# Kernel tuning notes

Measured on AMD Instinct MI355X. Metric: run time of the kernel, lower is better.

The kernel has to match this reference:

```python
import jax, jax.numpy as jnp
import numpy as np

EPS = 1e-5
RADIUS = 1.0

def bn(x, gamma, beta, axis=1):
    # inference-mode BatchNorm1d: running_mean=0, running_var=1
    shape = [1] * x.ndim
    shape[axis] = -1
    return x * (gamma / jnp.sqrt(1.0 + EPS)).reshape(shape) + beta.reshape(shape)

def pconv(x, w):
    # pointwise Conv1d (kernel_size=1): x [B,Cin,N], w [Cout,Cin]
    return jnp.einsum('oi,bin->bon', w, x)

def sq_dist(a, b):
    # a [B,N,3], b [B,S,3] -> squared pairwise distances [B,N,S]
    return (jnp.sum(a * a, -1)[:, :, None] + jnp.sum(b * b, -1)[:, None, :]
            - 2.0 * jnp.einsum('bnc,bsc->bns', a, b))

def index_points(points, idx):
    # points [B,S,...], idx [B,...] -> gathered [B, idx.shape[1:], ...]
    return jax.vmap(lambda p, i: p[i])(points, idx)

def fps(xyz, npoint):
    # farthest point sampling (deterministic start at index 0)
    B, N, _ = xyz.shape
    binds = jnp.arange(B)
    def step(carry, _):
        dist, far = carry
        c = xyz[binds, far]                                    # [B,3]
        d = jnp.sum((xyz - c[:, None, :]) ** 2, -1)            # [B,N]
        dist = jnp.minimum(dist, d)
        nxt = jnp.argmax(dist, -1).astype(jnp.int32)
        return (dist, nxt), far
    init = (jnp.full((B, N), 1e10, xyz.dtype), jnp.zeros((B,), jnp.int32))
    _, idx = jax.lax.scan(step, init, None, length=npoint)
    return jnp.transpose(idx)                                   # [B,npoint]

def query_ball(radius, nsample, xyz, new_xyz):
    # indices of first nsample points within radius of each center
    B, N, _ = xyz.shape
    S = new_xyz.shape[1]
    d2 = sq_dist(new_xyz, xyz)                                  # [B,S,N]
    gidx = jnp.broadcast_to(jnp.arange(N, dtype=jnp.int32), (B, S, N))
    gidx = jnp.where(d2 > radius * radius, N, gidx)
    gidx = jnp.sort(gidx, axis=-1)[:, :, :nsample]
    first = gidx[:, :, :1]
    gidx = jnp.where(gidx == N, first, gidx)
    return jnp.clip(gidx, 0, N - 1)

def sample_and_group(npoint, nsample, radius, xyz, points):
    fps_idx = fps(xyz, npoint)
    new_xyz = index_points(xyz, fps_idx)                        # [B,S,3]
    new_pts = index_points(points, fps_idx)                     # [B,S,D]
    idx = query_ball(radius, nsample, xyz, new_xyz)             # [B,S,K]
    grouped = index_points(points, idx)                         # [B,S,K,D]
    centered = grouped - new_pts[:, :, None, :]
    rep = jnp.broadcast_to(new_pts[:, :, None, :], centered.shape)
    return new_xyz, jnp.concatenate([centered, rep], axis=-1)   # [B,S,K,2D]

def local_op(x, w1, g1, b1, w2, g2, b2):
    # x [B,n,K,d]; shared pointwise MLP over channels then max over K
    h = jnp.einsum('oi,bnki->bnok', w1, x)
    h = jax.nn.relu(bn(h, g1, b1, axis=2))
    h = jnp.einsum('oi,bnik->bnok', w2, h)
    h = jax.nn.relu(bn(h, g2, b2, axis=2))
    return jnp.transpose(jnp.max(h, -1), (0, 2, 1))             # [B,out,n]

def feature_prop(xyz1, xyz2, points1, points2, w1, g1, b1, w2, g2, b2):
    # 3-NN inverse-distance interpolation of points2 onto xyz1, concat points1
    p1 = jnp.transpose(xyz1, (0, 2, 1))                         # [B,N,3]
    p2 = jnp.transpose(xyz2, (0, 2, 1))                         # [B,S,3]
    f2 = jnp.transpose(points2, (0, 2, 1))                      # [B,S,D2]
    negd, idx = jax.lax.top_k(-sq_dist(p1, p2), 3)              # [B,N,3]
    recip = 1.0 / (-negd + 1e-8)
    w = recip / jnp.sum(recip, -1, keepdims=True)
    interp = jnp.sum(index_points(f2, idx) * w[..., None], 2)   # [B,N,D2]
    new = jnp.concatenate([points1, jnp.transpose(interp, (0, 2, 1))], axis=1)
    new = jax.nn.relu(bn(pconv(new, w1), g1, b1))
    new = jax.nn.relu(bn(pconv(new, w2), g2, b2))
    return new


def setup_inputs() -> dict:
    key = jax.random.key(0)
    ks = iter(jax.random.split(key, 80))
    def W(*s):  return jax.random.normal(next(ks), s, jnp.float32) * 0.05
    def G(n):   return 1.0 + 0.1 * jax.random.normal(next(ks), (n,), jnp.float32)
    def Bt(n):  return 0.1 * jax.random.normal(next(ks), (n,), jnp.float32)
    inp = {"x": jax.random.uniform(next(ks), (4, 8192, 3), jnp.float32)}
    inp.update(w_emb1=W(64, 3), g_emb1=G(64), be_emb1=Bt(64),
               w_emb2=W(64, 64), g_emb2=G(64), be_emb2=Bt(64),
               l0_w1=W(128, 128), l0_g1=G(128), l0_b1=Bt(128),
               l0_w2=W(128, 128), l0_g2=G(128), l0_b2=Bt(128),
               l1_w1=W(256, 256), l1_g1=G(256), l1_b1=Bt(256),
               l1_w2=W(256, 256), l1_g2=G(256), l1_b2=Bt(256),
               f0_w1=W(256, 384), f0_g1=G(256), f0_b1=Bt(256),
               f0_w2=W(512, 256), f0_g2=G(512), f0_b2=Bt(512),
               f1_w1=W(512, 576), f1_g1=G(512), f1_b1=Bt(512),
               f1_w2=W(1024, 512), f1_g2=G(1024), f1_b2=Bt(1024),
               c1_w=W(512, 1024), c1_bias=Bt(512), c1_g=G(512), c1_beta=Bt(512),
               c2_w=W(128, 512), c2_bias=Bt(128), c2_g=G(128), c2_beta=Bt(128),
               out_w=W(8, 128), out_bias=Bt(8))
    return inp


def reference(x, w_emb1, g_emb1, be_emb1, w_emb2, g_emb2, be_emb2,
              l0_w1, l0_g1, l0_b1, l0_w2, l0_g2, l0_b2,
              l1_w1, l1_g1, l1_b1, l1_w2, l1_g2, l1_b2,
              f0_w1, f0_g1, f0_b1, f0_w2, f0_g2, f0_b2,
              f1_w1, f1_g1, f1_b1, f1_w2, f1_g2, f1_b2,
              c1_w, c1_bias, c1_g, c1_beta, c2_w, c2_bias, c2_g, c2_beta,
              out_w, out_bias):
    xyz = x                                                     # [B,N,3]
    h = jnp.transpose(x, (0, 2, 1))                             # [B,3,N]
    h = jax.nn.relu(bn(pconv(h, w_emb1), g_emb1, be_emb1))
    h = jax.nn.relu(bn(pconv(h, w_emb2), g_emb2, be_emb2))
    feats0 = h                                                  # [B,64,N]
    xyz1, g1f = sample_and_group(2048, 32, RADIUS, xyz, jnp.transpose(h, (0, 2, 1)))
    feats1 = local_op(g1f, l0_w1, l0_g1, l0_b1, l0_w2, l0_g2, l0_b2)   # [B,128,2048]
    xyz2, g2f = sample_and_group(1024, 32, RADIUS, xyz1, jnp.transpose(feats1, (0, 2, 1)))
    feats2 = local_op(g2f, l1_w1, l1_g1, l1_b1, l1_w2, l1_g2, l1_b2)   # [B,256,1024]
    h = feature_prop(jnp.transpose(xyz1, (0, 2, 1)), jnp.transpose(xyz2, (0, 2, 1)),
                     feats1, feats2, f0_w1, f0_g1, f0_b1, f0_w2, f0_g2, f0_b2)   # [B,512,2048]
    h = feature_prop(jnp.transpose(xyz, (0, 2, 1)), jnp.transpose(xyz1, (0, 2, 1)),
                     feats0, h, f1_w1, f1_g1, f1_b1, f1_w2, f1_g2, f1_b2)        # [B,1024,N]
    h = jax.nn.relu(bn(pconv(h, c1_w) + c1_bias[None, :, None], c1_g, c1_beta))
    h = jax.nn.relu(bn(pconv(h, c2_w) + c2_bias[None, :, None], c2_g, c2_beta))
    logits = pconv(h, out_w) + out_bias[None, :, None]
    return jnp.transpose(logits, (0, 2, 1))                     # [B,N,labels]
```

## Files before the change

kernel.cpp:

```cpp
#include <hip/hip_runtime.h>
#include <math.h>


static constexpr size_t O_FEATS0 = 0;
static constexpr size_t O_FEATS1 = 8388608;
static constexpr size_t O_FEATS2 = 12582912;
static constexpr size_t O_FP0OUT = 16777216;
static constexpr size_t O_XYZ1   = 33554432;
static constexpr size_t O_XYZ2   = 33652736;
static constexpr size_t O_FPS1   = 33701888;
static constexpr size_t O_FPS2   = 33734656;
static constexpr size_t O_BALL1  = 33751040;
static constexpr size_t O_BALL2  = 34799616;
static constexpr size_t O_NN0I   = 35323904;
static constexpr size_t O_NN0W   = 35422208;
static constexpr size_t O_NN1I   = 35520512;
static constexpr size_t O_NN1W   = 35913728;
static constexpr size_t O_REG0   = 36306944;
static constexpr size_t O_REG1   = 103415808;
static constexpr size_t WS_NEED  = 170524672;

typedef float v2f __attribute__((ext_vector_type(2)));

__device__ __forceinline__ unsigned long long u64max(unsigned long long a,
                                                     unsigned long long b) {
  return a > b ? a : b;
}
template <int CTRL>
__device__ __forceinline__ unsigned long long dpp_step(unsigned long long k) {
  const int lo = (int)(unsigned)k;
  const int hi = (int)(unsigned)(k >> 32);
  const int nlo = __builtin_amdgcn_update_dpp(lo, lo, CTRL, 0xf, 0xf, false);
  const int nhi = __builtin_amdgcn_update_dpp(hi, hi, CTRL, 0xf, 0xf, false);
  return ((unsigned long long)(unsigned)nhi << 32) | (unsigned)nlo;
}

template <int N, int NP>
__device__ void fps_core(const float* __restrict__ xyz, int* __restrict__ out,
                         float* __restrict__ oxyz, float* sx, float* sy,
                         float* sz, int* sfar, unsigned long long* skey,
                         int b, int t) {
  #pragma clang fp contract(off)
  constexpr int PPT = N / 256;
  constexpr int PAIRS = PPT / 2;
  const float* xb = xyz + (size_t)b * N * 3;
  for (int i = t; i < N; i += 256) {
    sx[i] = xb[i * 3 + 0];
    sy[i] = xb[i * 3 + 1];
    sz[i] = xb[i * 3 + 2];
  }
  __syncthreads();
  v2f px[PAIRS], py[PAIRS], pz[PAIRS], ds[PAIRS];
  #pragma unroll
  for (int k = 0; k < PAIRS; ++k) {
    const int g = t * PPT + 2 * k;
    px[k].x = sx[g]; px[k].y = sx[g + 1];
    py[k].x = sy[g]; py[k].y = sy[g + 1];
    pz[k].x = sz[g]; pz[k].y = sz[g + 1];
    ds[k].x = 1e10f; ds[k].y = 1e10f;
  }
  const int wid = t >> 6, lane = t & 63;
  int far = 0;
  float ccx = sx[0], ccy = sy[0], ccz = sz[0];
  for (int it = 0; it < NP; ++it) {
    if (t == 0) sfar[it] = far;
    v2f cx2, cy2, cz2;
    cx2.x = ccx; cx2.y = ccx;
    cy2.x = ccy; cy2.y = ccy;
    cz2.x = ccz; cz2.y = ccz;
    #pragma unroll
    for (int k = 0; k < PAIRS; ++k) {
      const v2f dx = px[k] - cx2;
      const v2f dy = py[k] - cy2;
      const v2f dz = pz[k] - cz2;
      const v2f d = dx * dx + dy * dy + dz * dz;
      v2f nd;
      nd.x = fminf(ds[k].x, d.x);
      nd.y = fminf(ds[k].y, d.y);
      ds[k] = nd;
    }
    v2f tv[PAIRS / 2];
    #pragma unroll
    for (int k = 0; k < PAIRS / 2; ++k) {
      tv[k].x = fmaxf(ds[k].x, ds[k + PAIRS / 2].x);
      tv[k].y = fmaxf(ds[k].y, ds[k + PAIRS / 2].y);
    }
    #pragma unroll
    for (int w = PAIRS / 4; w >= 1; w >>= 1) {
      #pragma unroll
      for (int k = 0; k < w; ++k) {
        tv[k].x = fmaxf(tv[k].x, tv[k + w].x);
        tv[k].y = fmaxf(tv[k].y, tv[k + w].y);
      }
    }
    const float bv = fmaxf(tv[0].x, tv[0].y);
    unsigned mask = 0u;
    #pragma unroll
    for (int k = 0; k < PAIRS; ++k) {
      mask |= (ds[k].x == bv) ? (1u << (2 * k)) : 0u;
      mask |= (ds[k].y == bv) ? (1u << (2 * k + 1)) : 0u;
    }
    const int bjl = __builtin_ctz(mask);
    unsigned long long bk =
        ((unsigned long long)__float_as_uint(bv) << 32) |
        (unsigned long long)(unsigned)(~(unsigned)(t * PPT + bjl));
    bk = u64max(bk, dpp_step<0x111>(bk));
    bk = u64max(bk, dpp_step<0x112>(bk));
    bk = u64max(bk, dpp_step<0x114>(bk));
    bk = u64max(bk, dpp_step<0x118>(bk));
    bk = u64max(bk, dpp_step<0x142>(bk));
    bk = u64max(bk, dpp_step<0x143>(bk));
    const int p = it & 1;
    if (lane == 63) skey[p * 4 + wid] = bk;
    __syncthreads();
    unsigned long long wk = skey[p * 4 + 0];
    #pragma unroll
    for (int q = 1; q < 4; ++q) {
      const unsigned long long k2 = skey[p * 4 + q];
      wk = (k2 > wk) ? k2 : wk;
    }
    far = (int)(~(unsigned)wk);
    ccx = sx[far]; ccy = sy[far]; ccz = sz[far];
  }
  __syncthreads();
  for (int i = t; i < NP; i += 256) {
    const int n = sfar[i];
    out[(size_t)b * NP + i] = n;
    oxyz[((size_t)b * NP + i) * 3 + 0] = sx[n];
    oxyz[((size_t)b * NP + i) * 3 + 1] = sy[n];
    oxyz[((size_t)b * NP + i) * 3 + 2] = sz[n];
  }
}

template <int N, int NP>
__global__ __launch_bounds__(256, 1) void fps_emb_kernel(
    const float* __restrict__ xyz, int* __restrict__ out,
    float* __restrict__ oxyz, const float* __restrict__ w1,
    const float* __restrict__ g1, const float* __restrict__ b1,
    const float* __restrict__ w2, const float* __restrict__ g2,
    const float* __restrict__ b2, float* __restrict__ femb) {
  __shared__ float sx[N], sy[N], sz[N];
  __shared__ int sfar[NP];
  __shared__ unsigned long long skey[8];
  if (blockIdx.x >= 4) {
    const int bid = blockIdx.x - 4;
    const int t = threadIdx.x;
    const int o = t & 63, pl = t >> 6;
    const int pt = bid * 4 + pl;
    const float x0 = xyz[(size_t)pt * 3 + 0];
    const float x1 = xyz[(size_t)pt * 3 + 1];
    const float x2 = xyz[(size_t)pt * 3 + 2];
    const float SQ = sqrtf(1.0f + 1e-5f);
    float v = w1[o * 3 + 0] * x0 + w1[o * 3 + 1] * x1 + w1[o * 3 + 2] * x2;
    v = fmaxf(v * (g1[o] / SQ) + b1[o], 0.0f);
    float* h = sx;
    h[pl * 64 + o] = v;
    __syncthreads();
    float acc = 0.0f;
    #pragma unroll 8
    for (int i = 0; i < 64; ++i) acc += w2[o * 64 + i] * h[pl * 64 + i];
    float y = fmaxf(acc * (g2[o] / SQ) + b2[o], 0.0f);
    femb[(size_t)pt * 64 + o] = y;
    return;
  }
  fps_core<N, NP>(xyz, out, oxyz, sx, sy, sz, sfar, skey, blockIdx.x,
                  threadIdx.x);
}

__global__ __launch_bounds__(256, 1) void ballnnfps_kernel(
    const float* __restrict__ cloud, const float* __restrict__ ctr,
    int* __restrict__ ballOut, int sbits, int N, int nBallBlk,
    const float* __restrict__ txyz, const float* __restrict__ sxyz,
    int* __restrict__ oi, float* __restrict__ ow, int s1bits, int S2,
    const float* __restrict__ fxyz, int* __restrict__ fout,
    float* __restrict__ foxyz) {
  __shared__ __align__(16) char smem[28800];
  const int t = threadIdx.x;
  if ((int)blockIdx.x < 4) {
    unsigned long long* skey = (unsigned long long*)smem;
    int* sfar = (int*)(smem + 64);
    float* sx = (float*)(smem + 64 + 4096);
    float* sy = sx + 2048;
    float* sz = sy + 2048;
    fps_core<2048, 1024>(fxyz, fout, foxyz, sx, sy, sz, sfar, skey,
                         blockIdx.x, t);
    return;
  }
  if ((int)blockIdx.x < 4 + nBallBlk) {
    int* lists = (int*)smem;
    const int lane = t & 63, wid = t >> 6;
    const int wg = (blockIdx.x - 4) * 4 + wid;
    const int b = wg >> sbits;
    const float cx = ctr[(size_t)wg * 3 + 0];
    const float cy = ctr[(size_t)wg * 3 + 1];
    const float cz = ctr[(size_t)wg * 3 + 2];
    const float an = __fadd_rn(__fadd_rn(__fmul_rn(cx, cx), __fmul_rn(cy, cy)),
                               __fmul_rn(cz, cz));
    int fill = 0;
    for (int ch = 0; ch < (N >> 6) && fill < 32; ++ch) {
      const int n = ch * 64 + lane;
      const float bx = cloud[((size_t)b * N + n) * 3 + 0];
      const float by = cloud[((size_t)b * N + n) * 3 + 1];
      const float bz = cloud[((size_t)b * N + n) * 3 + 2];
      const float bb = __fadd_rn(
          __fadd_rn(__fmul_rn(bx, bx), __fmul_rn(by, by)), __fmul_rn(bz, bz));
      const float dot = __fadd_rn(
          __fadd_rn(__fmul_rn(cx, bx), __fmul_rn(cy, by)), __fmul_rn(cz, bz));
      const float d2 = __fsub_rn(__fadd_rn(an, bb), __fmul_rn(2.0f, dot));
      const bool q = (d2 <= 1.0f);
      const unsigned long long mask = __ballot(q);
      if (q) {
        const int pos = fill + __popcll(mask & ((1ull << lane) - 1ull));
        if (pos < 32) lists[wid * 32 + pos] = n;
      }
      fill += (int)__popcll(mask);
    }
    __syncthreads();
    if (lane < 32) {
      int v = lists[wid * 32 + 0];
      if (lane < fill) v = lists[wid * 32 + lane];
      ballOut[(size_t)wg * 32 + lane] = v;
    }
    return;
  }
  float* ss = (float*)smem;
  const int row = (blockIdx.x - 4 - nBallBlk) * 256 + t;
  const int b = row >> s1bits;
  for (int i = t; i < S2 * 3; i += 256) ss[i] = sxyz[(size_t)b * S2 * 3 + i];
  __syncthreads();
  const float ax = txyz[(size_t)row * 3 + 0];
  const float ay = txyz[(size_t)row * 3 + 1];
  const float az = txyz[(size_t)row * 3 + 2];
  const float an = __fadd_rn(__fadd_rn(__fmul_rn(ax, ax), __fmul_rn(ay, ay)),
                             __fmul_rn(az, az));
  float d0 = 3.4e38f, d1 = 3.4e38f, d2v = 3.4e38f;
  int i0 = 0, i1 = 0, i2 = 0;
  for (int j = 0; j < S2; ++j) {
    const float bx = ss[j * 3 + 0], by = ss[j * 3 + 1], bz = ss[j * 3 + 2];
    const float bb = __fadd_rn(__fadd_rn(__fmul_rn(bx, bx), __fmul_rn(by, by)),
                               __fmul_rn(bz, bz));
    const float dot = __fadd_rn(__fadd_rn(__fmul_rn(ax, bx), __fmul_rn(ay, by)),
                                __fmul_rn(az, bz));
    const float dd = __fsub_rn(__fadd_rn(an, bb), __fmul_rn(2.0f, dot));
    if (dd < d0) {
      d2v = d1; i2 = i1; d1 = d0; i1 = i0; d0 = dd; i0 = j;
    } else if (dd < d1) {
      d2v = d1; i2 = i1; d1 = dd; i1 = j;
    } else if (dd < d2v) {
      d2v = dd; i2 = j;
    }
  }
  const float r0 = 1.0f / (d0 + 1e-8f);
  const float r1 = 1.0f / (d1 + 1e-8f);
  const float r2 = 1.0f / (d2v + 1e-8f);
  const float sum = __fadd_rn(__fadd_rn(r0, r1), r2);
  oi[(size_t)row * 3 + 0] = i0;
  oi[(size_t)row * 3 + 1] = i1;
  oi[(size_t)row * 3 + 2] = i2;
  ow[(size_t)row * 3 + 0] = r0 / sum;
  ow[(size_t)row * 3 + 1] = r1 / sum;
  ow[(size_t)row * 3 + 2] = r2 / sum;
}

__global__ __launch_bounds__(256) void ballnn_kernel(
    const float* __restrict__ cloud, const float* __restrict__ ctr,
    int* __restrict__ ballOut, int sbits, int N, int nBallBlk,
    const float* __restrict__ txyz, const float* __restrict__ sxyz,
    int* __restrict__ oi, float* __restrict__ ow, int s1bits, int S2) {
  __shared__ int lists[4][32];
  __shared__ float ss[6144];
  const int t = threadIdx.x;
  if ((int)blockIdx.x < nBallBlk) {
    const int lane = t & 63, wid = t >> 6;
    const int wg = blockIdx.x * 4 + wid;
    const int b = wg >> sbits;
    const float cx = ctr[(size_t)wg * 3 + 0];
    const float cy = ctr[(size_t)wg * 3 + 1];
    const float cz = ctr[(size_t)wg * 3 + 2];
    const float an = __fadd_rn(__fadd_rn(__fmul_rn(cx, cx), __fmul_rn(cy, cy)),
                               __fmul_rn(cz, cz));
    int fill = 0;
    for (int ch = 0; ch < (N >> 6) && fill < 32; ++ch) {
      const int n = ch * 64 + lane;
      const float bx = cloud[((size_t)b * N + n) * 3 + 0];
      const float by = cloud[((size_t)b * N + n) * 3 + 1];
      const float bz = cloud[((size_t)b * N + n) * 3 + 2];
      const float bb = __fadd_rn(
          __fadd_rn(__fmul_rn(bx, bx), __fmul_rn(by, by)), __fmul_rn(bz, bz));
      const float dot = __fadd_rn(
          __fadd_rn(__fmul_rn(cx, bx), __fmul_rn(cy, by)), __fmul_rn(cz, bz));
      const float d2 = __fsub_rn(__fadd_rn(an, bb), __fmul_rn(2.0f, dot));
      const bool q = (d2 <= 1.0f);
      const unsigned long long mask = __ballot(q);
      if (q) {
        const int pos = fill + __popcll(mask & ((1ull << lane) - 1ull));
        if (pos < 32) lists[wid][pos] = n;
      }
      fill += (int)__popcll(mask);
    }
    __syncthreads();
    if (lane < 32) {
      int v = lists[wid][0];
      if (lane < fill) v = lists[wid][lane];
      ballOut[(size_t)wg * 32 + lane] = v;
    }
    return;
  }
  const int row = (blockIdx.x - nBallBlk) * 256 + t;
  const int b = row >> s1bits;
  for (int i = t; i < S2 * 3; i += 256) ss[i] = sxyz[(size_t)b * S2 * 3 + i];
  __syncthreads();
  const float ax = txyz[(size_t)row * 3 + 0];
  const float ay = txyz[(size_t)row * 3 + 1];
  const float az = txyz[(size_t)row * 3 + 2];
  const float an = __fadd_rn(__fadd_rn(__fmul_rn(ax, ax), __fmul_rn(ay, ay)),
                             __fmul_rn(az, az));
  float d0 = 3.4e38f, d1 = 3.4e38f, d2v = 3.4e38f;
  int i0 = 0, i1 = 0, i2 = 0;
  for (int j = 0; j < S2; ++j) {
    const float bx = ss[j * 3 + 0], by = ss[j * 3 + 1], bz = ss[j * 3 + 2];
    const float bb = __fadd_rn(__fadd_rn(__fmul_rn(bx, bx), __fmul_rn(by, by)),
                               __fmul_rn(bz, bz));
    const float dot = __fadd_rn(__fadd_rn(__fmul_rn(ax, bx), __fmul_rn(ay, by)),
                                __fmul_rn(az, bz));
    const float dd = __fsub_rn(__fadd_rn(an, bb), __fmul_rn(2.0f, dot));
    if (dd < d0) {
      d2v = d1; i2 = i1; d1 = d0; i1 = i0; d0 = dd; i0 = j;
    } else if (dd < d1) {
      d2v = d1; i2 = i1; d1 = dd; i1 = j;
    } else if (dd < d2v) {
      d2v = dd; i2 = j;
    }
  }
  const float r0 = 1.0f / (d0 + 1e-8f);
  const float r1 = 1.0f / (d1 + 1e-8f);
  const float r2 = 1.0f / (d2v + 1e-8f);
  const float sum = __fadd_rn(__fadd_rn(r0, r1), r2);
  oi[(size_t)row * 3 + 0] = i0;
  oi[(size_t)row * 3 + 1] = i1;
  oi[(size_t)row * 3 + 2] = i2;
  ow[(size_t)row * 3 + 0] = r0 / sum;
  ow[(size_t)row * 3 + 1] = r1 / sum;
  ow[(size_t)row * 3 + 2] = r2 / sum;
}

#define CMAP(c) ((((c) >> 3) * 12) + ((c) & 7))

__global__ __launch_bounds__(256) void conv_gather_kernel(
    const float* __restrict__ f, const int* __restrict__ ball,
    const int* __restrict__ fps, int g0, int Cf, int sbits, int Npts,
    const float* __restrict__ W, float* __restrict__ Y, int O,
    const float* __restrict__ gamma, const float* __restrict__ beta) {
  const int C = Cf * 2;
  __shared__ float Xs[16][188];
  __shared__ float Ws[16][188];
  const int t = threadIdx.x;
  const size_t m0 = (size_t)blockIdx.x * 128;
  const int o0 = blockIdx.y * 128;
  const int r0 = t >> 2;
  const int cq0 = (t & 3) * 4;
  const int mq = t & 15, nq = t >> 4;
  const int ca = CMAP(r0), cb = CMAP(r0 + 64);
  const int mA = (int)m0 + r0, mB = (int)m0 + r0 + 64;
  const int glA = g0 + (mA >> 5), glB = g0 + (mB >> 5);
  const int srcA = ball[(size_t)glA * 32 + (mA & 31)];
  const int srcB = ball[(size_t)glB * 32 + (mB & 31)];
  const int ctrA = fps[glA], ctrB = fps[glB];
  const float* fbA = f + (size_t)(glA >> sbits) * Npts * Cf;
  const float* fbB = f + (size_t)(glB >> sbits) * Npts * Cf;
  v2f acc[8][4];
  #pragma unroll
  for (int i = 0; i < 8; ++i)
    #pragma unroll
    for (int j = 0; j < 4; ++j) acc[i][j] = (v2f){0.0f, 0.0f};

  for (int kk = 0; kk < C; kk += 16) {
    const int col = kk + cq0;
    const bool lo = col < Cf;
    const int col2 = lo ? col : col - Cf;
    float4 xa, xb;
    {
      const float4 c4 = *(const float4*)(fbA + (size_t)ctrA * Cf + col2);
      if (lo) {
        const float4 s4 = *(const float4*)(fbA + (size_t)srcA * Cf + col);
        xa = make_float4(s4.x - c4.x, s4.y - c4.y, s4.z - c4.z, s4.w - c4.w);
      } else {
        xa = c4;
      }
    }
    {
      const float4 c4 = *(const float4*)(fbB + (size_t)ctrB * Cf + col2);
      if (lo) {
        const float4 s4 = *(const float4*)(fbB + (size_t)srcB * Cf + col);
        xb = make_float4(s4.x - c4.x, s4.y - c4.y, s4.z - c4.z, s4.w - c4.w);
      } else {
        xb = c4;
      }
    }
    const float4 wa = *(const float4*)(W + (size_t)(o0 + r0) * C + kk + cq0);
    const float4 wb =
        *(const float4*)(W + (size_t)(o0 + r0 + 64) * C + kk + cq0);
    __syncthreads();
    Xs[cq0 + 0][ca] = xa.x; Xs[cq0 + 1][ca] = xa.y;
    Xs[cq0 + 2][ca] = xa.z; Xs[cq0 + 3][ca] = xa.w;
    Xs[cq0 + 0][cb] = xb.x; Xs[cq0 + 1][cb] = xb.y;
    Xs[cq0 + 2][cb] = xb.z; Xs[cq0 + 3][cb] = xb.w;
    Ws[cq0 + 0][ca] = wa.x; Ws[cq0 + 1][ca] = wa.y;
    Ws[cq0 + 2][ca] = wa.z; Ws[cq0 + 3][ca] = wa.w;
    Ws[cq0 + 0][cb] = wb.x; Ws[cq0 + 1][cb] = wb.y;
    Ws[cq0 + 2][cb] = wb.z; Ws[cq0 + 3][cb] = wb.w;
    __syncthreads();
    #pragma unroll
    for (int k = 0; k < 16; ++k) {
      const float4 a0 = *(const float4*)&Xs[k][mq * 12];
      const float4 a1 = *(const float4*)&Xs[k][mq * 12 + 4];
      const float4 b0 = *(const float4*)&Ws[k][nq * 12];
      const float4 b1 = *(const float4*)&Ws[k][nq * 12 + 4];
      const float am[8] = {a0.x, a0.y, a0.z, a0.w, a1.x, a1.y, a1.z, a1.w};
      v2f bv[4];
      bv[0] = (v2f){b0.x, b0.y};
      bv[1] = (v2f){b0.z, b0.w};
      bv[2] = (v2f){b1.x, b1.y};
      bv[3] = (v2f){b1.z, b1.w};
      #pragma unroll
      for (int i = 0; i < 8; ++i) {
        const v2f as = (v2f){am[i], am[i]};
        #pragma unroll
        for (int j = 0; j < 4; ++j) acc[i][j] += as * bv[j];
      }
    }
  }

  const float SQ = sqrtf(1.0f + 1e-5f);
  float s[8], sh[8];
  #pragma unroll
  for (int j = 0; j < 8; ++j) {
    const int o = o0 + nq * 8 + j;
    s[j] = gamma[o] / SQ;
    sh[j] = beta[o];
  }
  #pragma unroll
  for (int i = 0; i < 8; ++i) {
    float y[8];
    #pragma unroll
    for (int j = 0; j < 4; ++j) {
      y[2 * j] = fmaxf(acc[i][j].x * s[2 * j] + sh[2 * j], 0.0f);
      y[2 * j + 1] = fmaxf(acc[i][j].y * s[2 * j + 1] + sh[2 * j + 1], 0.0f);
    }
    const size_t off = (m0 + mq * 8 + i) * O + o0 + nq * 8;
    *(float4*)(Y + off) = make_float4(y[0], y[1], y[2], y[3]);
    *(float4*)(Y + off + 4) = make_float4(y[4], y[5], y[6], y[7]);
  }
}

__global__ __launch_bounds__(256) void conv2sm_kernel(
    const float* __restrict__ X, const float* __restrict__ W,
    float* __restrict__ F, int C, int O, const float* __restrict__ gamma,
    const float* __restrict__ beta) {
  __shared__ float Xs[16][188];
  __shared__ float Ws[16][188];
  const int t = threadIdx.x;
  const size_t m0 = (size_t)blockIdx.x * 128;
  const int o0 = blockIdx.y * 128;
  const int r0 = t >> 2;
  const int cq0 = (t & 3) * 4;
  const int mq = t & 15, nq = t >> 4;
  const int ca = CMAP(r0), cb = CMAP(r0 + 64);
  v2f acc[8][4];
  #pragma unroll
  for (int i = 0; i < 8; ++i)
    #pragma unroll
    for (int j = 0; j < 4; ++j) acc[i][j] = (v2f){0.0f, 0.0f};

  for (int kk = 0; kk < C; kk += 16) {
    const float4 xa = *(const float4*)(X + (m0 + r0) * C + kk + cq0);
    const float4 xb = *(const float4*)(X + (m0 + r0 + 64) * C + kk + cq0);
    const float4 wa = *(const float4*)(W + (size_t)(o0 + r0) * C + kk + cq0);
    const float4 wb =
        *(const float4*)(W + (size_t)(o0 + r0 + 64) * C + kk + cq0);
    __syncthreads();
    Xs[cq0 + 0][ca] = xa.x; Xs[cq0 + 1][ca] = xa.y;
    Xs[cq0 + 2][ca] = xa.z; Xs[cq0 + 3][ca] = xa.w;
    Xs[cq0 + 0][cb] = xb.x; Xs[cq0 + 1][cb] = xb.y;
    Xs[cq0 + 2][cb] = xb.z; Xs[cq0 + 3][cb] = xb.w;
    Ws[cq0 + 0][ca] = wa.x; Ws[cq0 + 1][ca] = wa.y;
    Ws[cq0 + 2][ca] = wa.z; Ws[cq0 + 3][ca] = wa.w;
    Ws[cq0 + 0][cb] = wb.x; Ws[cq0 + 1][cb] = wb.y;
    Ws[cq0 + 2][cb] = wb.z; Ws[cq0 + 3][cb] = wb.w;
    __syncthreads();
    #pragma unroll
    for (int k = 0; k < 16; ++k) {
      const float4 a0 = *(const float4*)&Xs[k][mq * 12];
      const float4 a1 = *(const float4*)&Xs[k][mq * 12 + 4];
      const float4 b0 = *(const float4*)&Ws[k][nq * 12];
      const float4 b1 = *(const float4*)&Ws[k][nq * 12 + 4];
      const float am[8] = {a0.x, a0.y, a0.z, a0.w, a1.x, a1.y, a1.z, a1.w};
      v2f bv[4];
      bv[0] = (v2f){b0.x, b0.y};
      bv[1] = (v2f){b0.z, b0.w};
      bv[2] = (v2f){b1.x, b1.y};
      bv[3] = (v2f){b1.z, b1.w};
      #pragma unroll
      for (int i = 0; i < 8; ++i) {
        const v2f as = (v2f){am[i], am[i]};
        #pragma unroll
        for (int j = 0; j < 4; ++j) acc[i][j] += as * bv[j];
      }
    }
  }

  const float SQ = sqrtf(1.0f + 1e-5f);
  float s[8], sh[8];
  #pragma unroll
  for (int j = 0; j < 8; ++j) {
    const int o = o0 + nq * 8 + j;
    s[j] = gamma[o] / SQ;
    sh[j] = beta[o];
  }
  float colmax[8];
  #pragma unroll
  for (int j = 0; j < 8; ++j) colmax[j] = -3.4e38f;
  #pragma unroll
  for (int i = 0; i < 8; ++i) {
    #pragma unroll
    for (int j = 0; j < 4; ++j) {
      const float va = fmaxf(acc[i][j].x * s[2 * j] + sh[2 * j], 0.0f);
      const float vb = fmaxf(acc[i][j].y * s[2 * j + 1] + sh[2 * j + 1], 0.0f);
      colmax[2 * j] = fmaxf(colmax[2 * j], va);
      colmax[2 * j + 1] = fmaxf(colmax[2 * j + 1], vb);
    }
  }
  __syncthreads();
  float* smax = &Xs[0][0];
  #pragma unroll
  for (int j = 0; j < 8; ++j) smax[mq * 132 + nq * 8 + j] = colmax[j];
  __syncthreads();
  #pragma unroll
  for (int q = 0; q < 2; ++q) {
    const int idx = t + q * 256;
    const int g = idx >> 7;
    const int col = idx & 127;
    const float m =
        fmaxf(fmaxf(smax[(4 * g + 0) * 132 + col], smax[(4 * g + 1) * 132 + col]),
              fmaxf(smax[(4 * g + 2) * 132 + col], smax[(4 * g + 3) * 132 + col]));
    F[(size_t)(blockIdx.x * 4 + g) * O + o0 + col] = m;
  }
}

__global__ __launch_bounds__(256) void conv_kernel(
    const float* __restrict__ X, const float* __restrict__ W,
    float* __restrict__ Y, int C, int O, const float* __restrict__ gamma,
    const float* __restrict__ beta, const float* __restrict__ bias, int relu) {
  __shared__ float Xs[16][188];
  __shared__ float Ws[16][188];
  const int t = threadIdx.x;
  const size_t m0 = (size_t)blockIdx.x * 128;
  const int o0 = blockIdx.y * 128;
  const int r0 = t >> 2;
  const int cq0 = (t & 3) * 4;
  const int mq = t & 15, nq = t >> 4;
  const int ca = CMAP(r0), cb = CMAP(r0 + 64);
  v2f acc[8][4];
  #pragma unroll
  for (int i = 0; i < 8; ++i)
    #pragma unroll
    for (int j = 0; j < 4; ++j) acc[i][j] = (v2f){0.0f, 0.0f};

  for (int kk = 0; kk < C; kk += 16) {
    const float4 xa = *(const float4*)(X + (m0 + r0) * C + kk + cq0);
    const float4 xb = *(const float4*)(X + (m0 + r0 + 64) * C + kk + cq0);
    const float4 wa = *(const float4*)(W + (size_t)(o0 + r0) * C + kk + cq0);
    const float4 wb =
        *(const float4*)(W + (size_t)(o0 + r0 + 64) * C + kk + cq0);
    __syncthreads();
    Xs[cq0 + 0][ca] = xa.x; Xs[cq0 + 1][ca] = xa.y;
    Xs[cq0 + 2][ca] = xa.z; Xs[cq0 + 3][ca] = xa.w;
    Xs[cq0 + 0][cb] = xb.x; Xs[cq0 + 1][cb] = xb.y;
    Xs[cq0 + 2][cb] = xb.z; Xs[cq0 + 3][cb] = xb.w;
    Ws[cq0 + 0][ca] = wa.x; Ws[cq0 + 1][ca] = wa.y;
    Ws[cq0 + 2][ca] = wa.z; Ws[cq0 + 3][ca] = wa.w;
    Ws[cq0 + 0][cb] = wb.x; Ws[cq0 + 1][cb] = wb.y;
    Ws[cq0 + 2][cb] = wb.z; Ws[cq0 + 3][cb] = wb.w;
    __syncthreads();
    #pragma unroll
    for (int k = 0; k < 16; ++k) {
      const float4 a0 = *(const float4*)&Xs[k][mq * 12];
      const float4 a1 = *(const float4*)&Xs[k][mq * 12 + 4];
      const float4 b0 = *(const float4*)&Ws[k][nq * 12];
      const float4 b1 = *(const float4*)&Ws[k][nq * 12 + 4];
      const float am[8] = {a0.x, a0.y, a0.z, a0.w, a1.x, a1.y, a1.z, a1.w};
      v2f bv[4];
      bv[0] = (v2f){b0.x, b0.y};
      bv[1] = (v2f){b0.z, b0.w};
      bv[2] = (v2f){b1.x, b1.y};
      bv[3] = (v2f){b1.z, b1.w};
      #pragma unroll
      for (int i = 0; i < 8; ++i) {
        const v2f as = (v2f){am[i], am[i]};
        #pragma unroll
        for (int j = 0; j < 4; ++j) acc[i][j] += as * bv[j];
      }
    }
  }

  const float SQ = sqrtf(1.0f + 1e-5f);
  float s[8], sh[8];
  #pragma unroll
  for (int j = 0; j < 8; ++j) {
    const int o = o0 + nq * 8 + j;
    const float sc = gamma ? (gamma[o] / SQ) : 1.0f;
    float bb = beta ? beta[o] : 0.0f;
    if (bias) bb = bb + bias[o] * sc;
    s[j] = sc; sh[j] = bb;
  }
  #pragma unroll
  for (int i = 0; i < 8; ++i) {
    float y[8];
    #pragma unroll
    for (int j = 0; j < 4; ++j) {
      float va = acc[i][j].x * s[2 * j] + sh[2 * j];
      float vb = acc[i][j].y * s[2 * j + 1] + sh[2 * j + 1];
      y[2 * j] = relu ? fmaxf(va, 0.0f) : va;
      y[2 * j + 1] = relu ? fmaxf(vb, 0.0f) : vb;
    }
    const size_t off = (m0 + mq * 8 + i) * O + o0 + nq * 8;
    *(float4*)(Y + off) = make_float4(y[0], y[1], y[2], y[3]);
    *(float4*)(Y + off + 4) = make_float4(y[4], y[5], y[6], y[7]);
  }
}

template <int CT, int C0, int CS2>
__global__ __launch_bounds__(256) void concat_interp_kernel(
    float* __restrict__ dst, const float* __restrict__ srcA,
    const float* __restrict__ srcB, const int* __restrict__ idx,
    const float* __restrict__ w, int s1bits, int S2) {
  const int id = blockIdx.x * 256 + threadIdx.x;
  constexpr int CPR = CT / 4;
  const int row = id / CPR;
  const int c4 = (id - row * CPR) * 4;
  if (c4 < C0) {
    const float4 v = *(const float4*)(srcA + (size_t)row * C0 + c4);
    *(float4*)(dst + (size_t)row * CT + c4) = v;
  } else {
    const int b = row >> s1bits;
    const int cc = c4 - C0;
    const int j0 = idx[(size_t)row * 3 + 0];
    const int j1 = idx[(size_t)row * 3 + 1];
    const int j2 = idx[(size_t)row * 3 + 2];
    const float w0 = w[(size_t)row * 3 + 0];
    const float w1 = w[(size_t)row * 3 + 1];
    const float w2 = w[(size_t)row * 3 + 2];
    const float4 f0 = *(const float4*)(srcB + ((size_t)b * S2 + j0) * CS2 + cc);
    const float4 f1 = *(const float4*)(srcB + ((size_t)b * S2 + j1) * CS2 + cc);
    const float4 f2 = *(const float4*)(srcB + ((size_t)b * S2 + j2) * CS2 + cc);
    float4 v;
    v.x = f0.x * w0 + f1.x * w1 + f2.x * w2;
    v.y = f0.y * w0 + f1.y * w1 + f2.y * w2;
    v.z = f0.z * w0 + f1.z * w1 + f2.z * w2;
    v.w = f0.w * w0 + f1.w * w1 + f2.w * w2;
    *(float4*)(dst + (size_t)row * CT + c4) = v;
  }
}

__global__ __launch_bounds__(256) void outfinal_kernel(
    const float* __restrict__ X, const float* __restrict__ Wt,
    const float* __restrict__ bias, float* __restrict__ out) {
  __shared__ float Xs[32][132];
  const int t = threadIdx.x;
  const int p0 = blockIdx.x * 32;
  #pragma unroll
  for (int q = 0; q < 4; ++q) {
    const int id = t + q * 256;
    const int r = id >> 5, c4 = (id & 31) * 4;
    const float4 v = *(const float4*)(X + (size_t)(p0 + r) * 128 + c4);
    Xs[r][c4 + 0] = v.x; Xs[r][c4 + 1] = v.y;
    Xs[r][c4 + 2] = v.z; Xs[r][c4 + 3] = v.w;
  }
  __syncthreads();
  const int p = t >> 3, o = t & 7;
  float acc = 0.0f;
  #pragma unroll 8
  for (int i = 0; i < 128; ++i) acc += Wt[o * 128 + i] * Xs[p][i];
  out[(size_t)(p0 + p) * 8 + o] = acc + bias[o];
}

extern "C" void kernel_launch(void* const* d_in, const int* in_sizes, int n_in,
                              void* d_out, int out_size, void* d_ws,
                              size_t ws_size, hipStream_t stream) {
  const float* x       = (const float*)d_in[0];
  const float* w_emb1  = (const float*)d_in[1];
  const float* g_emb1  = (const float*)d_in[2];
  const float* be_emb1 = (const float*)d_in[3];
  const float* w_emb2  = (const float*)d_in[4];
  const float* g_emb2  = (const float*)d_in[5];
  const float* be_emb2 = (const float*)d_in[6];
  const float* l0_w1 = (const float*)d_in[7];
  const float* l0_g1 = (const float*)d_in[8];
  const float* l0_b1 = (const float*)d_in[9];
  const float* l0_w2 = (const float*)d_in[10];
  const float* l0_g2 = (const float*)d_in[11];
  const float* l0_b2 = (const float*)d_in[12];
  const float* l1_w1 = (const float*)d_in[13];
  const float* l1_g1 = (const float*)d_in[14];
  const float* l1_b1 = (const float*)d_in[15];
  const float* l1_w2 = (const float*)d_in[16];
  const float* l1_g2 = (const float*)d_in[17];
  const float* l1_b2 = (const float*)d_in[18];
  const float* f0_w1 = (const float*)d_in[19];
  const float* f0_g1 = (const float*)d_in[20];
  const float* f0_b1 = (const float*)d_in[21];
  const float* f0_w2 = (const float*)d_in[22];
  const float* f0_g2 = (const float*)d_in[23];
  const float* f0_b2 = (const float*)d_in[24];
  const float* f1_w1 = (const float*)d_in[25];
  const float* f1_g1 = (const float*)d_in[26];
  const float* f1_b1 = (const float*)d_in[27];
  const float* f1_w2 = (const float*)d_in[28];
  const float* f1_g2 = (const float*)d_in[29];
  const float* f1_b2 = (const float*)d_in[30];
  const float* c1_w    = (const float*)d_in[31];
  const float* c1_bias = (const float*)d_in[32];
  const float* c1_g    = (const float*)d_in[33];
  const float* c1_beta = (const float*)d_in[34];
  const float* c2_w    = (const float*)d_in[35];
  const float* c2_bias = (const float*)d_in[36];
  const float* c2_g    = (const float*)d_in[37];
  const float* c2_beta = (const float*)d_in[38];
  const float* out_w    = (const float*)d_in[39];
  const float* out_bias = (const float*)d_in[40];

  if (ws_size < WS_NEED) return;

  char* ws = (char*)d_ws;
  float* feats0 = (float*)(ws + O_FEATS0);
  float* feats1 = (float*)(ws + O_FEATS1);
  float* feats2 = (float*)(ws + O_FEATS2);
  float* fp0out = (float*)(ws + O_FP0OUT);
  float* xyz1   = (float*)(ws + O_XYZ1);
  float* xyz2   = (float*)(ws + O_XYZ2);
  int*   fps1   = (int*)(ws + O_FPS1);
  int*   fps2   = (int*)(ws + O_FPS2);
  int*   ball1  = (int*)(ws + O_BALL1);
  int*   ball2  = (int*)(ws + O_BALL2);
  int*   nn0i   = (int*)(ws + O_NN0I);
  float* nn0w   = (float*)(ws + O_NN0W);
  int*   nn1i   = (int*)(ws + O_NN1I);
  float* nn1w   = (float*)(ws + O_NN1W);
  float* REG0   = (float*)(ws + O_REG0);
  float* REG1   = (float*)(ws + O_REG1);
  float* outp   = (float*)d_out;
  hipStream_t s = stream;

  fps_emb_kernel<8192, 2048><<<4 + 8192, 256, 0, s>>>(
      x, fps1, xyz1, w_emb1, g_emb1, be_emb1, w_emb2, g_emb2, be_emb2, feats0);

  ballnnfps_kernel<<<4 + 2048 + 128, 256, 0, s>>>(
      x, xyz1, ball1, 11, 8192, 2048, x, xyz1, nn1i, nn1w, 13, 2048,
      xyz1, fps2, xyz2);

  for (int c = 0; c < 2; ++c) {
    conv_gather_kernel<<<dim3(1024, 1), 256, 0, s>>>(
        feats0, ball1, fps1, c * 4096, 64, 11, 8192, l0_w1, REG1, 128, l0_g1,
        l0_b1);
    conv2sm_kernel<<<dim3(1024, 1), 256, 0, s>>>(
        REG1, l0_w2, feats1 + (size_t)c * 4096 * 128, 128, 128, l0_g2, l0_b2);
  }

  ballnn_kernel<<<1024 + 32, 256, 0, s>>>(xyz1, xyz2, ball2, 10, 2048, 1024,
                                          xyz1, xyz2, nn0i, nn0w, 11, 1024);

  for (int c = 0; c < 2; ++c) {
    conv_gather_kernel<<<dim3(512, 2), 256, 0, s>>>(
        feats1, ball2, fps2, c * 2048, 128, 10, 2048, l1_w1, REG1, 256, l1_g1,
        l1_b1);
    conv2sm_kernel<<<dim3(512, 2), 256, 0, s>>>(
        REG1, l1_w2, feats2 + (size_t)c * 2048 * 256, 256, 256, l1_g2, l1_b2);
  }

  concat_interp_kernel<384, 128, 256><<<3072, 256, 0, s>>>(
      REG0, feats1, feats2, nn0i, nn0w, 11, 1024);
  conv_kernel<<<dim3(64, 2), 256, 0, s>>>(REG0, f0_w1, REG1, 384, 256, f0_g1,
                                          f0_b1, nullptr, 1);
  conv_kernel<<<dim3(64, 4), 256, 0, s>>>(REG1, f0_w2, fp0out, 256, 512, f0_g2,
                                          f0_b2, nullptr, 1);

  for (int b = 0; b < 4; b += 2) {
    concat_interp_kernel<576, 64, 512><<<9216, 256, 0, s>>>(
        REG0, feats0 + (size_t)b * 8192 * 64, fp0out + (size_t)b * 2048 * 512,
        nn1i + (size_t)b * 8192 * 3, nn1w + (size_t)b * 8192 * 3, 13, 2048);
    conv_kernel<<<dim3(128, 4), 256, 0, s>>>(REG0, f1_w1, REG1, 576, 512,
                                             f1_g1, f1_b1, nullptr, 1);
    conv_kernel<<<dim3(128, 8), 256, 0, s>>>(REG1, f1_w2, REG0, 512, 1024,
                                             f1_g2, f1_b2, nullptr, 1);
    conv_kernel<<<dim3(128, 4), 256, 0, s>>>(REG0, c1_w, REG1, 1024, 512,
                                             c1_g, c1_beta, c1_bias, 1);
    conv_kernel<<<dim3(128, 1), 256, 0, s>>>(REG1, c2_w, REG0, 512, 128,
                                             c2_g, c2_beta, c2_bias, 1);
    outfinal_kernel<<<512, 256, 0, s>>>(REG0, out_w, out_bias,
                                        outp + (size_t)b * 8192 * 8);
  }
}
```

Before: 4.618 ms.

## Double-buffer shared-memory tiles in the three GEMM conv kernels

The three tiled fp32 GEMM kernels (gather-conv, conv+max, plain conv) now keep two shared-memory tile buffers. The global loads for the next K-slice are issued before computing on the current one. This removes one __syncthreads per iteration and hides global load latency behind the FMA loop. In exchange, shared memory per block doubles to about 48KB and register pressure rises from holding the prefetched values, which can lower occupancy.

```diff
diff --git a/kernel.cpp b/kernel.cpp
--- a/kernel.cpp
+++ b/kernel.cpp
@@ -346,14 +346,45 @@
 
 #define CMAP(c) ((((c) >> 3) * 12) + ((c) & 7))
 
+#define STORE_TILE(B)                                                   \
+  Xs[B][cq0 + 0][ca] = xa.x; Xs[B][cq0 + 1][ca] = xa.y;                 \
+  Xs[B][cq0 + 2][ca] = xa.z; Xs[B][cq0 + 3][ca] = xa.w;                 \
+  Xs[B][cq0 + 0][cb] = xb.x; Xs[B][cq0 + 1][cb] = xb.y;                 \
+  Xs[B][cq0 + 2][cb] = xb.z; Xs[B][cq0 + 3][cb] = xb.w;                 \
+  Ws[B][cq0 + 0][ca] = wa.x; Ws[B][cq0 + 1][ca] = wa.y;                 \
+  Ws[B][cq0 + 2][ca] = wa.z; Ws[B][cq0 + 3][ca] = wa.w;                 \
+  Ws[B][cq0 + 0][cb] = wb.x; Ws[B][cq0 + 1][cb] = wb.y;                 \
+  Ws[B][cq0 + 2][cb] = wb.z; Ws[B][cq0 + 3][cb] = wb.w;
+
+#define COMPUTE_TILE(B)                                                 \
+  _Pragma("unroll")                                                     \
+  for (int k = 0; k < 16; ++k) {                                        \
+    const float4 a0 = *(const float4*)&Xs[B][k][mq * 12];               \
+    const float4 a1 = *(const float4*)&Xs[B][k][mq * 12 + 4];           \
+    const float4 b0 = *(const float4*)&Ws[B][k][nq * 12];               \
+    const float4 b1 = *(const float4*)&Ws[B][k][nq * 12 + 4];           \
+    const float am[8] = {a0.x, a0.y, a0.z, a0.w, a1.x, a1.y, a1.z, a1.w}; \
+    v2f bv[4];                                                          \
+    bv[0] = (v2f){b0.x, b0.y};                                          \
+    bv[1] = (v2f){b0.z, b0.w};                                          \
+    bv[2] = (v2f){b1.x, b1.y};                                          \
+    bv[3] = (v2f){b1.z, b1.w};                                          \
+    _Pragma("unroll")                                                   \
+    for (int i = 0; i < 8; ++i) {                                       \
+      const v2f as = (v2f){am[i], am[i]};                               \
+      _Pragma("unroll")                                                 \
+      for (int j = 0; j < 4; ++j) acc[i][j] += as * bv[j];              \
+    }                                                                   \
+  }
+
 __global__ __launch_bounds__(256) void conv_gather_kernel(
     const float* __restrict__ f, const int* __restrict__ ball,
     const int* __restrict__ fps, int g0, int Cf, int sbits, int Npts,
     const float* __restrict__ W, float* __restrict__ Y, int O,
     const float* __restrict__ gamma, const float* __restrict__ beta) {
   const int C = Cf * 2;
-  __shared__ float Xs[16][188];
-  __shared__ float Ws[16][188];
+  __shared__ float Xs[2][16][188];
+  __shared__ float Ws[2][16][188];
   const int t = threadIdx.x;
   const size_t m0 = (size_t)blockIdx.x * 128;
   const int o0 = blockIdx.y * 128;
@@ -374,62 +405,51 @@
     #pragma unroll
     for (int j = 0; j < 4; ++j) acc[i][j] = (v2f){0.0f, 0.0f};
 
+  float4 xa, xb, wa, wb;
+  #define GLOAD(kk)                                                          \
+    {                                                                        \
+      const int col = (kk) + cq0;                                            \
+      const bool lo = col < Cf;                                              \
+      const int col2 = lo ? col : col - Cf;                                  \
+      {                                                                      \
+        const float4 c4 = *(const float4*)(fbA + (size_t)ctrA * Cf + col2);  \
+        if (lo) {                                                            \
+          const float4 s4 = *(const float4*)(fbA + (size_t)srcA * Cf + col); \
+          xa = make_float4(s4.x - c4.x, s4.y - c4.y, s4.z - c4.z,            \
+                           s4.w - c4.w);                                     \
+        } else {                                                             \
+          xa = c4;                                                           \
+        }                                                                    \
+      }                                                                      \
+      {                                                                      \
+        const float4 c4 = *(const float4*)(fbB + (size_t)ctrB * Cf + col2);  \
+        if (lo) {                                                            \
+          const float4 s4 = *(const float4*)(fbB + (size_t)srcB * Cf + col); \
+          xb = make_float4(s4.x - c4.x, s4.y - c4.y, s4.z - c4.z,            \
+                           s4.w - c4.w);                                     \
+        } else {                                                             \
+          xb = c4;                                                           \
+        }                                                                    \
+      }                                                                      \
+      wa = *(const float4*)(W + (size_t)(o0 + r0) * C + (kk) + cq0);         \
+      wb = *(const float4*)(W + (size_t)(o0 + r0 + 64) * C + (kk) + cq0);    \
+    }
+
+  GLOAD(0)
+  STORE_TILE(0)
+  __syncthreads();
+  int cur = 0;
   for (int kk = 0; kk < C; kk += 16) {
-    const int col = kk + cq0;
-    const bool lo = col < Cf;
-    const int col2 = lo ? col : col - Cf;
-    float4 xa, xb;
-    {
-      const float4 c4 = *(const float4*)(fbA + (size_t)ctrA * Cf + col2);
-      if (lo) {
-        const float4 s4 = *(const float4*)(fbA + (size_t)srcA * Cf + col);
-        xa = make_float4(s4.x - c4.x, s4.y - c4.y, s4.z - c4.z, s4.w - c4.w);
-      } else {
-        xa = c4;
-      }
-    }
-    {
-      const float4 c4 = *(const float4*)(fbB + (size_t)ctrB * Cf + col2);
-      if (lo) {
-        const float4 s4 = *(const float4*)(fbB + (size_t)srcB * Cf + col);
-        xb = make_float4(s4.x - c4.x, s4.y - c4.y, s4.z - c4.z, s4.w - c4.w);
-      } else {
-        xb = c4;
-      }
-    }
-    const float4 wa = *(const float4*)(W + (size_t)(o0 + r0) * C + kk + cq0);
-    const float4 wb =
-        *(const float4*)(W + (size_t)(o0 + r0 + 64) * C + kk + cq0);
-    __syncthreads();
-    Xs[cq0 + 0][ca] = xa.x; Xs[cq0 + 1][ca] = xa.y;
-    Xs[cq0 + 2][ca] = xa.z; Xs[cq0 + 3][ca] = xa.w;
-    Xs[cq0 + 0][cb] = xb.x; Xs[cq0 + 1][cb] = xb.y;
-    Xs[cq0 + 2][cb] = xb.z; Xs[cq0 + 3][cb] = xb.w;
-    Ws[cq0 + 0][ca] = wa.x; Ws[cq0 + 1][ca] = wa.y;
-    Ws[cq0 + 2][ca] = wa.z; Ws[cq0 + 3][ca] = wa.w;
-    Ws[cq0 + 0][cb] = wb.x; Ws[cq0 + 1][cb] = wb.y;
-    Ws[cq0 + 2][cb] = wb.z; Ws[cq0 + 3][cb] = wb.w;
-    __syncthreads();
-    #pragma unroll
-    for (int k = 0; k < 16; ++k) {
-      const float4 a0 = *(const float4*)&Xs[k][mq * 12];
-      const float4 a1 = *(const float4*)&Xs[k][mq * 12 + 4];
-      const float4 b0 = *(const float4*)&Ws[k][nq * 12];
-      const float4 b1 = *(const float4*)&Ws[k][nq * 12 + 4];
-      const float am[8] = {a0.x, a0.y, a0.z, a0.w, a1.x, a1.y, a1.z, a1.w};
-      v2f bv[4];
-      bv[0] = (v2f){b0.x, b0.y};
-      bv[1] = (v2f){b0.z, b0.w};
-      bv[2] = (v2f){b1.x, b1.y};
-      bv[3] = (v2f){b1.z, b1.w};
-      #pragma unroll
-      for (int i = 0; i < 8; ++i) {
-        const v2f as = (v2f){am[i], am[i]};
-        #pragma unroll
-        for (int j = 0; j < 4; ++j) acc[i][j] += as * bv[j];
-      }
-    }
-  }
+    const bool nxt = (kk + 16) < C;
+    if (nxt) GLOAD(kk + 16)
+    COMPUTE_TILE(cur)
+    if (nxt) {
+      STORE_TILE(cur ^ 1)
+      __syncthreads();
+      cur ^= 1;
+    }
+  }
+  #undef GLOAD
 
   const float SQ = sqrtf(1.0f + 1e-5f);
   float s[8], sh[8];
@@ -457,8 +477,8 @@
     const float* __restrict__ X, const float* __restrict__ W,
     float* __restrict__ F, int C, int O, const float* __restrict__ gamma,
     const float* __restrict__ beta) {
-  __shared__ float Xs[16][188];
-  __shared__ float Ws[16][188];
+  __shared__ float Xs[2][16][188];
+  __shared__ float Ws[2][16][188];
   const int t = threadIdx.x;
   const size_t m0 = (size_t)blockIdx.x * 128;
   const int o0 = blockIdx.y * 128;
@@ -472,42 +492,30 @@
     #pragma unroll
     for (int j = 0; j < 4; ++j) acc[i][j] = (v2f){0.0f, 0.0f};
 
+  float4 xa, xb, wa, wb;
+  #define GLOAD(kk)                                                          \
+    {                                                                        \
+      xa = *(const float4*)(X + (m0 + r0) * C + (kk) + cq0);                 \
+      xb = *(const float4*)(X + (m0 + r0 + 64) * C + (kk) + cq0);            \
+      wa = *(const float4*)(W + (size_t)(o0 + r0) * C + (kk) + cq0);         \
+      wb = *(const float4*)(W + (size_t)(o0 + r0 + 64) * C + (kk) + cq0);    \
+    }
+
+  GLOAD(0)
+  STORE_TILE(0)
+  __syncthreads();
+  int cur = 0;
   for (int kk = 0; kk < C; kk += 16) {
-    const float4 xa = *(const float4*)(X + (m0 + r0) * C + kk + cq0);
-    const float4 xb = *(const float4*)(X + (m0 + r0 + 64) * C + kk + cq0);
-    const float4 wa = *(const float4*)(W + (size_t)(o0 + r0) * C + kk + cq0);
-    const float4 wb =
-        *(const float4*)(W + (size_t)(o0 + r0 + 64) * C + kk + cq0);
-    __syncthreads();
-    Xs[cq0 + 0][ca] = xa.x; Xs[cq0 + 1][ca] = xa.y;
-    Xs[cq0 + 2][ca] = xa.z; Xs[cq0 + 3][ca] = xa.w;
-    Xs[cq0 + 0][cb] = xb.x; Xs[cq0 + 1][cb] = xb.y;
-    Xs[cq0 + 2][cb] = xb.z; Xs[cq0 + 3][cb] = xb.w;
-    Ws[cq0 + 0][ca] = wa.x; Ws[cq0 + 1][ca] = wa.y;
-    Ws[cq0 + 2][ca] = wa.z; Ws[cq0 + 3][ca] = wa.w;
-    Ws[cq0 + 0][cb] = wb.x; Ws[cq0 + 1][cb] = wb.y;
-    Ws[cq0 + 2][cb] = wb.z; Ws[cq0 + 3][cb] = wb.w;
-    __syncthreads();
-    #pragma unroll
-    for (int k = 0; k < 16; ++k) {
-      const float4 a0 = *(const float4*)&Xs[k][mq * 12];
-      const float4 a1 = *(const float4*)&Xs[k][mq * 12 + 4];
-      const float4 b0 = *(const float4*)&Ws[k][nq * 12];
-      const float4 b1 = *(const float4*)&Ws[k][nq * 12 + 4];
-      const float am[8] = {a0.x, a0.y, a0.z, a0.w, a1.x, a1.y, a1.z, a1.w};
-      v2f bv[4];
-      bv[0] = (v2f){b0.x, b0.y};
-      bv[1] = (v2f){b0.z, b0.w};
-      bv[2] = (v2f){b1.x, b1.y};
-      bv[3] = (v2f){b1.z, b1.w};
-      #pragma unroll
-      for (int i = 0; i < 8; ++i) {
-        const v2f as = (v2f){am[i], am[i]};
-        #pragma unroll
-        for (int j = 0; j < 4; ++j) acc[i][j] += as * bv[j];
-      }
-    }
-  }
+    const bool nxt = (kk + 16) < C;
+    if (nxt) GLOAD(kk + 16)
+    COMPUTE_TILE(cur)
+    if (nxt) {
+      STORE_TILE(cur ^ 1)
+      __syncthreads();
+      cur ^= 1;
+    }
+  }
+  #undef GLOAD
 
   const float SQ = sqrtf(1.0f + 1e-5f);
   float s[8], sh[8];
@@ -531,7 +539,7 @@
     }
   }
   __syncthreads();
-  float* smax = &Xs[0][0];
+  float* smax = &Xs[0][0][0];
   #pragma unroll
   for (int j = 0; j < 8; ++j) smax[mq * 132 + nq * 8 + j] = colmax[j];
   __syncthreads();
@@ -551,8 +559,8 @@
     const float* __restrict__ X, const float* __restrict__ W,
     float* __restrict__ Y, int C, int O, const float* __restrict__ gamma,
     const float* __restrict__ beta, const float* __restrict__ bias, int relu) {
-  __shared__ float Xs[16][188];
-  __shared__ float Ws[16][188];
+  __shared__ float Xs[2][16][188];
+  __shared__ float Ws[2][16][188];
   const int t = threadIdx.x;
   const size_t m0 = (size_t)blockIdx.x * 128;
   const int o0 = blockIdx.y * 128;
@@ -566,42 +574,30 @@
     #pragma unroll
     for (int j = 0; j < 4; ++j) acc[i][j] = (v2f){0.0f, 0.0f};
 
+  float4 xa, xb, wa, wb;
+  #define GLOAD(kk)                                                          \
+    {                                                                        \
+      xa = *(const float4*)(X + (m0 + r0) * C + (kk) + cq0);                 \
+      xb = *(const float4*)(X + (m0 + r0 + 64) * C + (kk) + cq0);            \
+      wa = *(const float4*)(W + (size_t)(o0 + r0) * C + (kk) + cq0);         \
+      wb = *(const float4*)(W + (size_t)(o0 + r0 + 64) * C + (kk) + cq0);    \
+    }
+
+  GLOAD(0)
+  STORE_TILE(0)
+  __syncthreads();
+  int cur = 0;
   for (int kk = 0; kk < C; kk += 16) {
-    const float4 xa = *(const float4*)(X + (m0 + r0) * C + kk + cq0);
-    const float4 xb = *(const float4*)(X + (m0 + r0 + 64) * C + kk + cq0);
-    const float4 wa = *(const float4*)(W + (size_t)(o0 + r0) * C + kk + cq0);
-    const float4 wb =
-        *(const float4*)(W + (size_t)(o0 + r0 + 64) * C + kk + cq0);
-    __syncthreads();
-    Xs[cq0 + 0][ca] = xa.x; Xs[cq0 + 1][ca] = xa.y;
-    Xs[cq0 + 2][ca] = xa.z; Xs[cq0 + 3][ca] = xa.w;
-    Xs[cq0 + 0][cb] = xb.x; Xs[cq0 + 1][cb] = xb.y;
-    Xs[cq0 + 2][cb] = xb.z; Xs[cq0 + 3][cb] = xb.w;
-    Ws[cq0 + 0][ca] = wa.x; Ws[cq0 + 1][ca] = wa.y;
-    Ws[cq0 + 2][ca] = wa.z; Ws[cq0 + 3][ca] = wa.w;
-    Ws[cq0 + 0][cb] = wb.x; Ws[cq0 + 1][cb] = wb.y;
-    Ws[cq0 + 2][cb] = wb.z; Ws[cq0 + 3][cb] = wb.w;
-    __syncthreads();
-    #pragma unroll
-    for (int k = 0; k < 16; ++k) {
-      const float4 a0 = *(const float4*)&Xs[k][mq * 12];
-      const float4 a1 = *(const float4*)&Xs[k][mq * 12 + 4];
-      const float4 b0 = *(const float4*)&Ws[k][nq * 12];
-      const float4 b1 = *(const float4*)&Ws[k][nq * 12 + 4];
-      const float am[8] = {a0.x, a0.y, a0.z, a0.w, a1.x, a1.y, a1.z, a1.w};
-      v2f bv[4];
-      bv[0] = (v2f){b0.x, b0.y};
-      bv[1] = (v2f){b0.z, b0.w};
-      bv[2] = (v2f){b1.x, b1.y};
-      bv[3] = (v2f){b1.z, b1.w};
-      #pragma unroll
-      for (int i = 0; i < 8; ++i) {
-        const v2f as = (v2f){am[i], am[i]};
-        #pragma unroll
-        for (int j = 0; j < 4; ++j) acc[i][j] += as * bv[j];
-      }
-    }
-  }
+    const bool nxt = (kk + 16) < C;
+    if (nxt) GLOAD(kk + 16)
+    COMPUTE_TILE(cur)
+    if (nxt) {
+      STORE_TILE(cur ^ 1)
+      __syncthreads();
+      cur ^= 1;
+    }
+  }
+  #undef GLOAD
 
   const float SQ = sqrtf(1.0f + 1e-5f);
   float s[8], sh[8];
```

Measured after the change: 4.631 ms (median of 2 runs). No clear change (+0.3%).
